# Optimization experiments

Hardware: AMD Instinct MI355X
Metric: run time of the kernel (lower is better)

## Reference

```python
import jax, jax.numpy as jnp
import numpy as np

jax.config.update("jax_enable_x64", True)

DIM = 128          # state dimension
T = 4096           # number of time points
BATCH = 64         # batched initial conditions (columns of x0)
N_UPPER = DIM * (DIM - 1) // 2  # 8128


def setup_inputs() -> dict:
    key = jax.random.key(0)
    k1, k2 = jax.random.split(key)
    return {
        "t": jnp.arange(T, dtype=jnp.float64) * 0.01,               # uniform time grid
        "x0": jax.random.normal(k1, (DIM, BATCH), dtype=jnp.float64),
        "S_upper": jax.random.normal(k2, (N_UPPER,), dtype=jnp.float64) * 0.3,
        "D_raw": jnp.ones((DIM,), dtype=jnp.float64) * 0.1,
    }


def _get_A(S_upper, D_raw):
    # skew-symmetric S from upper-triangular entries, minus positive diagonal D
    iu, ju = np.triu_indices(DIM, k=1)  # static index sets
    S = jnp.zeros((DIM, DIM), dtype=S_upper.dtype).at[iu, ju].set(S_upper)
    S = S - S.T
    return S - jnp.diag(jax.nn.softplus(D_raw))


def reference(t, x0, S_upper, D_raw):
    A = _get_A(S_upper, D_raw)
    dt = t[1] - t[0]
    expAdt = jax.scipy.linalg.expm(A * dt)  # [DIM, DIM]

    def step(x, _):
        x = expAdt @ x  # [DIM, BATCH]
        return x, x

    _, ys = jax.lax.scan(step, x0, None, length=T - 1)  # [T-1, DIM, BATCH]
    return jnp.concatenate([x0[None], ys], axis=0)      # [T, DIM, BATCH]
```

## Files before the change

kernel.cpp:

```cpp
#include <hip/hip_runtime.h>
#include <math.h>

#define DIM 128
#define GP(s)    ((s) * 16384)
#define YOFFI    (65 * 16384)
#define XOFF(q)  ((97 + (q)) * 16384)
#define TOFF(i)  ((105 + (i) - 1) * 16384)
#define FWOFFI   (169 * 16384)
#define FYOFFI   (201 * 16384)
#define ALPHA    16.0f

typedef _Float16 f16x8 __attribute__((ext_vector_type(8)));
typedef float    f32x4 __attribute__((ext_vector_type(4)));

__device__ __forceinline__ float4 ld4(const float* p) { return *(const float4*)p; }

__device__ __forceinline__ void stageA(const float* __restrict__ A, float* AT, int tid)
{
    for (int idx = tid; idx < DIM * DIM; idx += 256)
        AT[(idx & 127) * 132 + (idx >> 7)] = A[idx];
}

__device__ __forceinline__ void mm_core(const float* AT, const float* Bs,
                                        float (&acc)[4][4], int tid)
{
    int d0 = (tid & 31) * 4, c0 = (tid >> 5) * 4;
    #pragma unroll 4
    for (int k = 0; k < DIM; k++) {
        float4 a4 = ld4(&AT[k * 132 + d0]);
        float4 b4 = ld4(&Bs[k * 36 + c0]);
        float a_[4] = {a4.x, a4.y, a4.z, a4.w};
        float b_[4] = {b4.x, b4.y, b4.z, b4.w};
        #pragma unroll
        for (int i = 0; i < 4; i++)
            #pragma unroll
            for (int j = 0; j < 4; j++) acc[i][j] += a_[i] * b_[j];
    }
}

__global__ __launch_bounds__(256) void k_x2(const float* __restrict__ t,
                                            const float* __restrict__ x0,
                                            const float* __restrict__ S,
                                            const float* __restrict__ D,
                                            float* __restrict__ ws)
{
    __shared__ __align__(16) float AT[DIM * 132];
    __shared__ __align__(16) float Bs[DIM * 36];
    int tid = threadIdx.x, bid = blockIdx.x, cpan = bid * 32;
    float sc = (t[1] - t[0]) * ALPHA;
    for (int e = tid; e < 16384; e += 256) {
        int r = e >> 7, c = e & 127;
        float a;
        if (r == c)      a = -log1pf(expf(D[r]));
        else if (r < c)  a =  S[(r * (2 * DIM - r - 1)) / 2 + (c - r - 1)];
        else             a = -S[(c * (2 * DIM - c - 1)) / 2 + (r - c - 1)];
        a *= sc;
        AT[c * 132 + r] = a;
        if (c >= cpan && c < cpan + 32) Bs[r * 36 + (c - cpan)] = a;
        if (bid == 0) ws[XOFF(0) + e] = a;
    }
    if (bid == 1) for (int e = tid; e < 8192; e += 256) ws[YOFFI + e] = x0[e];
    if (bid == 2) {
        _Float16* Wf = (_Float16*)(ws + FWOFFI);
        for (int ch = tid; ch < 2048; ch += 256) {
            int m = ch >> 4, k0 = (ch & 15) << 3;
            f16x8 hv;
            #pragma unroll
            for (int q = 0; q < 8; q++) hv[q] = (m == k0 + q) ? (_Float16)1.0f : (_Float16)0.0f;
            int lane = (m & 15) | (((k0 >> 3) & 3) << 4);
            size_t off = (((size_t)(m >> 4) * 4 + (k0 >> 5)) * 64 + lane) * 8;
            *(f16x8*)(Wf + off) = hv;
        }
    }
    if (bid == 3) {
        _Float16* Yf = (_Float16*)(ws + FYOFFI);
        for (int slot = tid; slot < 1024; slot += 256) {
            int ls = slot & 63, tile = slot >> 6;
            int n = (tile >> 2) * 16 + (ls & 15);
            int k0 = (tile & 3) * 32 + ((ls >> 4) & 3) * 8;
            f16x8 hv;
            #pragma unroll
            for (int q = 0; q < 8; q++) hv[q] = (_Float16)x0[(size_t)(k0 + q) * 64 + n];
            *(f16x8*)(Yf + (size_t)slot * 8) = hv;
        }
    }
    __syncthreads();
    float acc[4][4] = {};
    mm_core(AT, Bs, acc, tid);
    int d0 = (tid & 31) * 4, c0 = (tid >> 5) * 4;
    #pragma unroll
    for (int r = 0; r < 4; r++) {
        float4 st = make_float4(acc[r][0], acc[r][1], acc[r][2], acc[r][3]);
        *(float4*)&ws[XOFF(1) + (size_t)(d0 + r) * DIM + cpan + c0] = st;
    }
}

struct Jobs { int4 jb[33]; };

__global__ __launch_bounds__(256) void k_mm(float* __restrict__ ws, Jobs jobs)
{
    __shared__ __align__(16) _Float16 fB[2][16384];
    const int4 jb = jobs.jb[blockIdx.x];
    const int ncols = jb.w & 255;
    const int fragj = (jb.w >> 8) - 1;
    const float* A = ws + jb.x;
    const float* B = ws + jb.y;
    float* C = ws + jb.z;
    const int tid = threadIdx.x, wave = tid >> 6, lane = tid & 63;

    f16x8 ah[2][4], al[2][4];
    #pragma unroll
    for (int mt = 0; mt < 2; mt++)
        #pragma unroll
        for (int kc = 0; kc < 4; kc++) {
            int m = wave * 32 + mt * 16 + (lane & 15);
            int k0 = kc * 32 + ((lane >> 4) & 3) * 8;
            const float* src = A + (size_t)m * DIM + k0;
            float4 p = ld4(src), r = ld4(src + 4);
            float v[8] = {p.x, p.y, p.z, p.w, r.x, r.y, r.z, r.w};
            f16x8 h8, l8;
            #pragma unroll
            for (int q = 0; q < 8; q++) {
                _Float16 h = (_Float16)v[q];
                h8[q] = h; l8[q] = (_Float16)(v[q] - (float)h);
            }
            ah[mt][kc] = h8; al[mt][kc] = l8;
        }

    const int nslots = (DIM * ncols) >> 3;
    for (int slot = tid; slot < nslots; slot += 256) {
        int ls = slot & 63, tile = slot >> 6;
        int n = (tile >> 2) * 16 + (ls & 15);
        int k0 = (tile & 3) * 32 + ((ls >> 4) & 3) * 8;
        f16x8 h8, l8;
        #pragma unroll
        for (int q = 0; q < 8; q++) {
            float v = B[(size_t)(k0 + q) * ncols + n];
            _Float16 h = (_Float16)v;
            h8[q] = h; l8[q] = (_Float16)(v - (float)h);
        }
        *(f16x8*)&fB[0][(size_t)slot * 8] = h8;
        *(f16x8*)&fB[1][(size_t)slot * 8] = l8;
    }
    __syncthreads();

    const int NT = ncols >> 4;
    f32x4 acc[2][8] = {};
    for (int kc = 0; kc < 4; kc++) {
        #pragma unroll
        for (int nt = 0; nt < 8; nt++) {
            if (nt >= NT) break;
            size_t bo = ((size_t)(nt * 4 + kc) * 64 + lane) * 8;
            f16x8 bh = *(const f16x8*)&fB[0][bo];
            f16x8 bl = *(const f16x8*)&fB[1][bo];
            #pragma unroll
            for (int mt = 0; mt < 2; mt++) {
                acc[mt][nt] = __builtin_amdgcn_mfma_f32_16x16x32_f16(ah[mt][kc], bh, acc[mt][nt], 0, 0, 0);
                acc[mt][nt] = __builtin_amdgcn_mfma_f32_16x16x32_f16(ah[mt][kc], bl, acc[mt][nt], 0, 0, 0);
                acc[mt][nt] = __builtin_amdgcn_mfma_f32_16x16x32_f16(al[mt][kc], bh, acc[mt][nt], 0, 0, 0);
            }
        }
    }
    __syncthreads();

    float* Cst = (float*)&fB[0][0];
    #pragma unroll
    for (int mt = 0; mt < 2; mt++)
        #pragma unroll
        for (int nt = 0; nt < 8; nt++) {
            if (nt >= NT) break;
            int row = wave * 32 + mt * 16 + ((lane >> 4) << 2);
            int n = nt * 16 + (lane & 15);
            #pragma unroll
            for (int p = 0; p < 4; p++)
                Cst[(size_t)(row + p) * ncols + n] = acc[mt][nt][p];
        }
    __syncthreads();
    for (int e = tid * 4; e < DIM * ncols; e += 1024)
        *(float4*)&C[e] = ld4(&Cst[e]);
    if (fragj >= 0) {
        _Float16* Yf = (_Float16*)(ws + FYOFFI) + (size_t)fragj * 8192;
        for (int slot = tid; slot < 1024; slot += 256) {
            int ls = slot & 63, tile = slot >> 6;
            int n = (tile >> 2) * 16 + (ls & 15);
            int k0 = (tile & 3) * 32 + ((ls >> 4) & 3) * 8;
            f16x8 hv;
            #pragma unroll
            for (int q = 0; q < 8; q++) hv[q] = (_Float16)Cst[(size_t)(k0 + q) * 64 + n];
            *(f16x8*)(Yf + (size_t)slot * 8) = hv;
        }
    }
}

__global__ __launch_bounds__(256) void k_ps1(float* __restrict__ ws)
{
    __shared__ __align__(16) float AT[DIM * 132];
    __shared__ __align__(16) float Bs[DIM * 36];
    int i = blockIdx.x + 1, cpan = blockIdx.y * 32, tid = threadIdx.x;
    float r = (float)i / ALPHA;
    float c[24]; c[0] = 1.0f;
    #pragma unroll
    for (int n = 1; n < 24; n++) c[n] = c[n - 1] * (r / (float)n);
    stageA(ws + XOFF(7), AT, tid);
    for (int idx = tid; idx < DIM * 8; idx += 256) {
        int k = idx >> 3, cc4 = (idx & 7) * 4;
        float4 b = make_float4(0.f, 0.f, 0.f, 0.f);
        #pragma unroll
        for (int q = 1; q < 8; q++) {
            float4 x = ld4(&ws[XOFF(q - 1) + (size_t)k * DIM + cpan + cc4]);
            b.x += c[16 + q] * x.x; b.y += c[16 + q] * x.y;
            b.z += c[16 + q] * x.z; b.w += c[16 + q] * x.w;
        }
        int col = cpan + cc4;
        if (k >= col && k < col + 4) (&b.x)[k - col] += c[16];
        *(float4*)&Bs[k * 36 + cc4] = b;
    }
    __syncthreads();
    float acc[4][4] = {};
    mm_core(AT, Bs, acc, tid);
    int d0 = (tid & 31) * 4, c0 = (tid >> 5) * 4;
    float* T = ws + TOFF(i);
    #pragma unroll
    for (int rr = 0; rr < 4; rr++) {
        int dd = d0 + rr;
        float add[4] = {0.f, 0.f, 0.f, 0.f};
        #pragma unroll
        for (int q = 1; q < 8; q++) {
            float4 x = ld4(&ws[XOFF(q - 1) + (size_t)dd * DIM + cpan + c0]);
            add[0] += c[8 + q] * x.x; add[1] += c[8 + q] * x.y;
            add[2] += c[8 + q] * x.z; add[3] += c[8 + q] * x.w;
        }
        int col0 = cpan + c0;
        if (dd >= col0 && dd < col0 + 4) add[dd - col0] += c[8];
        float4 st = make_float4(acc[rr][0] + add[0], acc[rr][1] + add[1],
                                acc[rr][2] + add[2], acc[rr][3] + add[3]);
        *(float4*)&T[(size_t)dd * DIM + cpan + c0] = st;
    }
}

__global__ __launch_bounds__(256) void k_ps2(float* __restrict__ ws)
{
    __shared__ __align__(16) float AT[DIM * 132];
    __shared__ __align__(16) float Bs[DIM * 36];
    int i = blockIdx.x + 1, cpan = blockIdx.y * 32, tid = threadIdx.x;
    float r = (float)i / ALPHA;
    float c[8]; c[0] = 1.0f;
    #pragma unroll
    for (int n = 1; n < 8; n++) c[n] = c[n - 1] * (r / (float)n);
    stageA(ws + XOFF(7), AT, tid);
    const float* T = ws + TOFF(i);
    for (int idx = tid; idx < DIM * 32; idx += 256) {
        int k = idx >> 5, cc = idx & 31;
        Bs[k * 36 + cc] = T[(size_t)k * DIM + cpan + cc];
    }
    __syncthreads();
    float acc[4][4] = {};
    mm_core(AT, Bs, acc, tid);
    int d0 = (tid & 31) * 4, c0 = (tid >> 5) * 4;
    #pragma unroll
    for (int rr = 0; rr < 4; rr++) {
        int dd = d0 + rr;
        float add[4] = {0.f, 0.f, 0.f, 0.f};
        #pragma unroll
        for (int q = 1; q < 8; q++) {
            float4 x = ld4(&ws[XOFF(q - 1) + (size_t)dd * DIM + cpan + c0]);
            add[0] += c[q] * x.x; add[1] += c[q] * x.y;
            add[2] += c[q] * x.z; add[3] += c[q] * x.w;
        }
        int col0 = cpan + c0;
        if (dd >= col0 && dd < col0 + 4) add[dd - col0] += 1.0f;
        #pragma unroll
        for (int j = 0; j < 4; j++) acc[rr][j] += add[j];
    }
    if (i == 64) {
        float* G = ws + GP(0);
        #pragma unroll
        for (int rr = 0; rr < 4; rr++) {
            float4 st = make_float4(acc[rr][0], acc[rr][1], acc[rr][2], acc[rr][3]);
            *(float4*)&G[(size_t)(d0 + rr) * DIM + cpan + c0] = st;
        }
        return;
    }
    __syncthreads();
    #pragma unroll
    for (int rr = 0; rr < 4; rr++)
        #pragma unroll
        for (int j = 0; j < 4; j++) Bs[(d0 + rr) * 36 + c0 + j] = acc[rr][j];
    __syncthreads();
    _Float16* Wf = (_Float16*)(ws + FWOFFI);
    for (int ch = tid; ch < 512; ch += 256) {
        int m = ch >> 2, k0l = (ch & 3) * 8, k0 = cpan + k0l;
        f16x8 hv;
        #pragma unroll
        for (int q = 0; q < 8; q++) hv[q] = (_Float16)Bs[m * 36 + k0l + q];
        int lane = (m & 15) | (((k0 >> 3) & 3) << 4);
        size_t off = (size_t)i * 16384 + (((size_t)(m >> 4) * 4 + (k0 >> 5)) * 64 + lane) * 8;
        *(f16x8*)(Wf + off) = hv;
    }
}

__global__ __launch_bounds__(256) void k_final(const _Float16* __restrict__ Wf,
                                               const _Float16* __restrict__ Yf,
                                               float* __restrict__ out)
{
    int i = blockIdx.x, j = blockIdx.y;
    int tid = threadIdx.x, wave = tid >> 6, lane = tid & 63;
    const _Float16* Ab = Yf + (size_t)j * 8192;
    const _Float16* Bb = Wf + (size_t)i * 16384;
    f32x4 acc[4][2] = {};
    #pragma unroll
    for (int ks = 0; ks < 4; ks++) {
        f16x8 a[4], b[2];
        #pragma unroll
        for (int bt = 0; bt < 4; bt++)
            a[bt] = *(const f16x8*)(Ab + (((size_t)bt * 4 + ks) * 64 + lane) * 8);
        #pragma unroll
        for (int nn = 0; nn < 2; nn++)
            b[nn] = *(const f16x8*)(Bb + (((size_t)(wave * 2 + nn) * 4 + ks) * 64 + lane) * 8);
        #pragma unroll
        for (int bt = 0; bt < 4; bt++)
            #pragma unroll
            for (int nn = 0; nn < 2; nn++)
                acc[bt][nn] = __builtin_amdgcn_mfma_f32_16x16x32_f16(a[bt], b[nn], acc[bt][nn], 0, 0, 0);
    }
    float* slab = out + (size_t)(j * 64 + i) * 8192;
    int nlo = lane & 15, b0 = (lane >> 4) * 4;
    #pragma unroll
    for (int bt = 0; bt < 4; bt++)
        #pragma unroll
        for (int nn = 0; nn < 2; nn++) {
            int n = (wave * 2 + nn) * 16 + nlo;
            __builtin_nontemporal_store(acc[bt][nn],
                (f32x4*)&slab[(size_t)n * 64 + bt * 16 + b0]);
        }
}

static inline void addjob(Jobs& J, int& n, int a, int b, int c, int ncols, int fragj)
{
    J.jb[n++] = make_int4(a, b, c, ncols | ((fragj + 1) << 8));
}

extern "C" void kernel_launch(void* const* d_in, const int* in_sizes, int n_in,
                              void* d_out, int out_size, void* d_ws, size_t ws_size,
                              hipStream_t stream)
{
    const float* t  = (const float*)d_in[0];
    const float* x0 = (const float*)d_in[1];
    const float* S  = (const float*)d_in[2];
    const float* D  = (const float*)d_in[3];
    float* out = (float*)d_out;
    float* ws  = (float*)d_ws;
    _Float16* Wf = (_Float16*)(ws + FWOFFI);
    _Float16* Yf = (_Float16*)(ws + FYOFFI);

    hipLaunchKernelGGL(k_x2, dim3(4), dim3(256), 0, stream, t, x0, S, D, ws);

    Jobs J; int n;
    n = 0;
    addjob(J, n, XOFF(1), XOFF(0), XOFF(2), 128, -1);
    addjob(J, n, XOFF(1), XOFF(1), XOFF(3), 128, -1);
    hipLaunchKernelGGL(k_mm, dim3(n), dim3(256), 0, stream, ws, J);
    n = 0;
    for (int q = 1; q <= 4; q++) addjob(J, n, XOFF(3), XOFF(q - 1), XOFF(3 + q), 128, -1);
    hipLaunchKernelGGL(k_mm, dim3(n), dim3(256), 0, stream, ws, J);

    hipLaunchKernelGGL(k_ps1, dim3(64, 4), dim3(256), 0, stream, ws);
    hipLaunchKernelGGL(k_ps2, dim3(64, 4), dim3(256), 0, stream, ws);

    n = 0;
    addjob(J, n, GP(0), GP(0), GP(1), 128, -1);
    addjob(J, n, GP(0), YOFFI, YOFFI + 8192, 64, 1);
    hipLaunchKernelGGL(k_mm, dim3(n), dim3(256), 0, stream, ws, J);
    n = 0;
    addjob(J, n, GP(1), GP(1), GP(2), 128, -1);
    addjob(J, n, GP(1), YOFFI,        YOFFI + 2 * 8192, 64, 2);
    addjob(J, n, GP(1), YOFFI + 8192, YOFFI + 3 * 8192, 64, 3);
    hipLaunchKernelGGL(k_mm, dim3(n), dim3(256), 0, stream, ws, J);
    n = 0;
    addjob(J, n, GP(2), GP(2), GP(3), 128, -1);
    for (int jj = 0; jj < 4; jj++)
        addjob(J, n, GP(2), YOFFI + jj * 8192, YOFFI + (4 + jj) * 8192, 64, 4 + jj);
    hipLaunchKernelGGL(k_mm, dim3(n), dim3(256), 0, stream, ws, J);
    n = 0;
    addjob(J, n, GP(3), GP(3), GP(4), 128, -1);
    for (int jj = 0; jj < 8; jj++)
        addjob(J, n, GP(3), YOFFI + jj * 8192, YOFFI + (8 + jj) * 8192, 64, 8 + jj);
    hipLaunchKernelGGL(k_mm, dim3(n), dim3(256), 0, stream, ws, J);
    n = 0;
    addjob(J, n, GP(4), GP(4), GP(5), 128, -1);
    for (int jj = 0; jj < 16; jj++)
        addjob(J, n, GP(4), YOFFI + jj * 8192, YOFFI + (16 + jj) * 8192, 64, 16 + jj);
    hipLaunchKernelGGL(k_mm, dim3(n), dim3(256), 0, stream, ws, J);
    n = 0;
    for (int jj = 0; jj < 32; jj++)
        addjob(J, n, GP(5), YOFFI + jj * 8192, YOFFI + (32 + jj) * 8192, 64, 32 + jj);
    hipLaunchKernelGGL(k_mm, dim3(n), dim3(256), 0, stream, ws, J);

    hipLaunchKernelGGL(k_final, dim3(64, 64), dim3(256), 0, stream, Wf, Yf, out);
}
```

Baseline: 218.1 us.

## Keep transposed copies of matrices so MFMA B fragments load directly from global

Replaces the k_mm kernel with k_atom, which reads the B operand from a pre-transposed matrix in global memory and splits it into fp16 hi/lo fragments in registers. This removes the LDS staging pass and its barrier. Each square product also writes its transpose, and the state propagation is reformulated as Y^T·G^T so that each job computes a 64x128 tile with the state as the A operand. The cost is extra transposed writes and strided global reads per fragment, in exchange for fewer LDS round trips and fewer synchronisations per job.

```diff
diff --git a/kernel.cpp b/kernel.cpp
--- a/kernel.cpp
+++ b/kernel.cpp
@@ -3,17 +3,30 @@
 
 #define DIM 128
 #define GP(s)    ((s) * 16384)
-#define YOFFI    (65 * 16384)
-#define XOFF(q)  ((97 + (q)) * 16384)
-#define TOFF(i)  ((105 + (i) - 1) * 16384)
-#define FWOFFI   (169 * 16384)
-#define FYOFFI   (201 * 16384)
+#define GTP(s)   ((6 + (s)) * 16384)
+#define YP(j)    (13 * 16384 + (j) * 8192)
+#define XOFF(q)  ((44 + (q)) * 16384)
+#define XTOFF(q) ((52 + (q)) * 16384)
+#define TOFF(i)  ((60 + (i)) * 16384)
+#define FWOFFI   (125 * 16384)
+#define FYOFFI   (157 * 16384)
 #define ALPHA    16.0f
 
 typedef _Float16 f16x8 __attribute__((ext_vector_type(8)));
 typedef float    f32x4 __attribute__((ext_vector_type(4)));
 
 __device__ __forceinline__ float4 ld4(const float* p) { return *(const float4*)p; }
+
+__device__ __forceinline__ void splitv(const float* src, f16x8& h8, f16x8& l8)
+{
+    float4 p = ld4(src), r = ld4(src + 4);
+    float v[8] = {p.x, p.y, p.z, p.w, r.x, r.y, r.z, r.w};
+    #pragma unroll
+    for (int q = 0; q < 8; q++) {
+        _Float16 h = (_Float16)v[q];
+        h8[q] = h; l8[q] = (_Float16)(v[q] - (float)h);
+    }
+}
 
 __device__ __forceinline__ void stageA(const float* __restrict__ A, float* AT, int tid)
 {
@@ -57,22 +70,13 @@
         a *= sc;
         AT[c * 132 + r] = a;
         if (c >= cpan && c < cpan + 32) Bs[r * 36 + (c - cpan)] = a;
-        if (bid == 0) ws[XOFF(0) + e] = a;
-    }
-    if (bid == 1) for (int e = tid; e < 8192; e += 256) ws[YOFFI + e] = x0[e];
-    if (bid == 2) {
-        _Float16* Wf = (_Float16*)(ws + FWOFFI);
-        for (int ch = tid; ch < 2048; ch += 256) {
-            int m = ch >> 4, k0 = (ch & 15) << 3;
-            f16x8 hv;
-            #pragma unroll
-            for (int q = 0; q < 8; q++) hv[q] = (m == k0 + q) ? (_Float16)1.0f : (_Float16)0.0f;
-            int lane = (m & 15) | (((k0 >> 3) & 3) << 4);
-            size_t off = (((size_t)(m >> 4) * 4 + (k0 >> 5)) * 64 + lane) * 8;
-            *(f16x8*)(Wf + off) = hv;
-        }
-    }
-    if (bid == 3) {
+        if (bid == 0) { ws[XOFF(1) + e] = a; ws[XTOFF(1) + c * DIM + r] = a; }
+    }
+    if (bid == 1) {
+        for (int e = tid; e < 8192; e += 256) {
+            int b = e >> 7, d = e & 127;
+            ws[YP(0) + e] = x0[(size_t)d * 64 + b];
+        }
         _Float16* Yf = (_Float16*)(ws + FYOFFI);
         for (int slot = tid; slot < 1024; slot += 256) {
             int ls = slot & 63, tile = slot >> 6;
@@ -84,6 +88,18 @@
             *(f16x8*)(Yf + (size_t)slot * 8) = hv;
         }
     }
+    if (bid == 2) {
+        _Float16* Wf = (_Float16*)(ws + FWOFFI);
+        for (int ch = tid; ch < 2048; ch += 256) {
+            int m = ch >> 4, k0 = (ch & 15) << 3;
+            f16x8 hv;
+            #pragma unroll
+            for (int q = 0; q < 8; q++) hv[q] = (m == k0 + q) ? (_Float16)1.0f : (_Float16)0.0f;
+            int lane = (m & 15) | (((k0 >> 3) & 3) << 4);
+            size_t off = (((size_t)(m >> 4) * 4 + (k0 >> 5)) * 64 + lane) * 8;
+            *(f16x8*)(Wf + off) = hv;
+        }
+    }
     __syncthreads();
     float acc[4][4] = {};
     mm_core(AT, Bs, acc, tid);
@@ -91,102 +107,90 @@
     #pragma unroll
     for (int r = 0; r < 4; r++) {
         float4 st = make_float4(acc[r][0], acc[r][1], acc[r][2], acc[r][3]);
-        *(float4*)&ws[XOFF(1) + (size_t)(d0 + r) * DIM + cpan + c0] = st;
-    }
-}
-
-struct Jobs { int4 jb[33]; };
-
-__global__ __launch_bounds__(256) void k_mm(float* __restrict__ ws, Jobs jobs)
-{
-    __shared__ __align__(16) _Float16 fB[2][16384];
-    const int4 jb = jobs.jb[blockIdx.x];
-    const int ncols = jb.w & 255;
-    const int fragj = (jb.w >> 8) - 1;
-    const float* A = ws + jb.x;
-    const float* B = ws + jb.y;
-    float* C = ws + jb.z;
+        *(float4*)&ws[XOFF(2) + (size_t)(d0 + r) * DIM + cpan + c0] = st;
+        #pragma unroll
+        for (int j = 0; j < 4; j++)
+            ws[XTOFF(2) + (size_t)(cpan + c0 + j) * DIM + d0 + r] = acc[r][j];
+    }
+}
+
+struct AJobs { int4 a[32]; int aux[32]; };
+
+__global__ __launch_bounds__(256) void k_atom(float* __restrict__ ws, AJobs JB)
+{
+    __shared__ __align__(16) float Cst[DIM * 133];
     const int tid = threadIdx.x, wave = tid >> 6, lane = tid & 63;
+    const int4 jb = JB.a[blockIdx.x];
+    const int aux = JB.aux[blockIdx.x];
+    const int type = jb.w;
+    const float* A  = ws + jb.x;
+    const float* Bt = ws + jb.y;
+    float* C        = ws + jb.z;
+    const int nmt = (type == 0) ? 2 : 1;
+    const int mlane = lane & 15, koct = (lane >> 4) & 3;
 
     f16x8 ah[2][4], al[2][4];
     #pragma unroll
-    for (int mt = 0; mt < 2; mt++)
+    for (int mt = 0; mt < 2; mt++) {
+        if (mt >= nmt) break;
         #pragma unroll
         for (int kc = 0; kc < 4; kc++) {
-            int m = wave * 32 + mt * 16 + (lane & 15);
-            int k0 = kc * 32 + ((lane >> 4) & 3) * 8;
-            const float* src = A + (size_t)m * DIM + k0;
-            float4 p = ld4(src), r = ld4(src + 4);
-            float v[8] = {p.x, p.y, p.z, p.w, r.x, r.y, r.z, r.w};
-            f16x8 h8, l8;
-            #pragma unroll
-            for (int q = 0; q < 8; q++) {
-                _Float16 h = (_Float16)v[q];
-                h8[q] = h; l8[q] = (_Float16)(v[q] - (float)h);
-            }
-            ah[mt][kc] = h8; al[mt][kc] = l8;
-        }
-
-    const int nslots = (DIM * ncols) >> 3;
-    for (int slot = tid; slot < nslots; slot += 256) {
-        int ls = slot & 63, tile = slot >> 6;
-        int n = (tile >> 2) * 16 + (ls & 15);
-        int k0 = (tile & 3) * 32 + ((ls >> 4) & 3) * 8;
-        f16x8 h8, l8;
-        #pragma unroll
-        for (int q = 0; q < 8; q++) {
-            float v = B[(size_t)(k0 + q) * ncols + n];
-            _Float16 h = (_Float16)v;
-            h8[q] = h; l8[q] = (_Float16)(v - (float)h);
-        }
-        *(f16x8*)&fB[0][(size_t)slot * 8] = h8;
-        *(f16x8*)&fB[1][(size_t)slot * 8] = l8;
-    }
-    __syncthreads();
-
-    const int NT = ncols >> 4;
+            int m = (wave * nmt + mt) * 16 + mlane;
+            splitv(A + (size_t)m * DIM + kc * 32 + koct * 8, ah[mt][kc], al[mt][kc]);
+        }
+    }
     f32x4 acc[2][8] = {};
     for (int kc = 0; kc < 4; kc++) {
         #pragma unroll
         for (int nt = 0; nt < 8; nt++) {
-            if (nt >= NT) break;
-            size_t bo = ((size_t)(nt * 4 + kc) * 64 + lane) * 8;
-            f16x8 bh = *(const f16x8*)&fB[0][bo];
-            f16x8 bl = *(const f16x8*)&fB[1][bo];
+            int n = nt * 16 + mlane;
+            f16x8 bh, bl;
+            splitv(Bt + (size_t)n * DIM + kc * 32 + koct * 8, bh, bl);
             #pragma unroll
             for (int mt = 0; mt < 2; mt++) {
+                if (mt >= nmt) break;
                 acc[mt][nt] = __builtin_amdgcn_mfma_f32_16x16x32_f16(ah[mt][kc], bh, acc[mt][nt], 0, 0, 0);
                 acc[mt][nt] = __builtin_amdgcn_mfma_f32_16x16x32_f16(ah[mt][kc], bl, acc[mt][nt], 0, 0, 0);
                 acc[mt][nt] = __builtin_amdgcn_mfma_f32_16x16x32_f16(al[mt][kc], bh, acc[mt][nt], 0, 0, 0);
             }
         }
     }
-    __syncthreads();
-
-    float* Cst = (float*)&fB[0][0];
-    #pragma unroll
-    for (int mt = 0; mt < 2; mt++)
+    #pragma unroll
+    for (int mt = 0; mt < 2; mt++) {
+        if (mt >= nmt) break;
         #pragma unroll
         for (int nt = 0; nt < 8; nt++) {
-            if (nt >= NT) break;
-            int row = wave * 32 + mt * 16 + ((lane >> 4) << 2);
-            int n = nt * 16 + (lane & 15);
-            #pragma unroll
-            for (int p = 0; p < 4; p++)
-                Cst[(size_t)(row + p) * ncols + n] = acc[mt][nt][p];
-        }
-    __syncthreads();
-    for (int e = tid * 4; e < DIM * ncols; e += 1024)
-        *(float4*)&C[e] = ld4(&Cst[e]);
-    if (fragj >= 0) {
-        _Float16* Yf = (_Float16*)(ws + FYOFFI) + (size_t)fragj * 8192;
+            int row = (wave * nmt + mt) * 16 + (lane >> 4) * 4;
+            int col = nt * 16 + mlane;
+            #pragma unroll
+            for (int p = 0; p < 4; p++) Cst[(size_t)(row + p) * 133 + col] = acc[mt][nt][p];
+        }
+    }
+    __syncthreads();
+    const int M = nmt * 64;
+    for (int e = tid * 4; e < M * DIM; e += 1024) {
+        int row = e >> 7, col = e & 127;
+        const float* s = &Cst[(size_t)row * 133 + col];
+        *(float4*)&C[e] = make_float4(s[0], s[1], s[2], s[3]);
+    }
+    if (type == 0) {
+        float* Ct = ws + aux;
+        for (int e = tid * 4; e < 16384; e += 1024) {
+            int crow = e >> 7, r0 = e & 127;
+            *(float4*)&Ct[e] = make_float4(Cst[(size_t)(r0 + 0) * 133 + crow],
+                                           Cst[(size_t)(r0 + 1) * 133 + crow],
+                                           Cst[(size_t)(r0 + 2) * 133 + crow],
+                                           Cst[(size_t)(r0 + 3) * 133 + crow]);
+        }
+    } else {
+        _Float16* Yf = (_Float16*)(ws + FYOFFI) + (size_t)aux * 8192;
         for (int slot = tid; slot < 1024; slot += 256) {
             int ls = slot & 63, tile = slot >> 6;
-            int n = (tile >> 2) * 16 + (ls & 15);
+            int m = (tile >> 2) * 16 + (ls & 15);
             int k0 = (tile & 3) * 32 + ((ls >> 4) & 3) * 8;
             f16x8 hv;
             #pragma unroll
-            for (int q = 0; q < 8; q++) hv[q] = (_Float16)Cst[(size_t)(k0 + q) * 64 + n];
+            for (int q = 0; q < 8; q++) hv[q] = (_Float16)Cst[(size_t)m * 133 + k0 + q];
             *(f16x8*)(Yf + (size_t)slot * 8) = hv;
         }
     }
@@ -201,13 +205,13 @@
     float c[24]; c[0] = 1.0f;
     #pragma unroll
     for (int n = 1; n < 24; n++) c[n] = c[n - 1] * (r / (float)n);
-    stageA(ws + XOFF(7), AT, tid);
+    stageA(ws + XOFF(8), AT, tid);
     for (int idx = tid; idx < DIM * 8; idx += 256) {
         int k = idx >> 3, cc4 = (idx & 7) * 4;
         float4 b = make_float4(0.f, 0.f, 0.f, 0.f);
         #pragma unroll
         for (int q = 1; q < 8; q++) {
-            float4 x = ld4(&ws[XOFF(q - 1) + (size_t)k * DIM + cpan + cc4]);
+            float4 x = ld4(&ws[XOFF(q) + (size_t)k * DIM + cpan + cc4]);
             b.x += c[16 + q] * x.x; b.y += c[16 + q] * x.y;
             b.z += c[16 + q] * x.z; b.w += c[16 + q] * x.w;
         }
@@ -226,7 +230,7 @@
         float add[4] = {0.f, 0.f, 0.f, 0.f};
         #pragma unroll
         for (int q = 1; q < 8; q++) {
-            float4 x = ld4(&ws[XOFF(q - 1) + (size_t)dd * DIM + cpan + c0]);
+            float4 x = ld4(&ws[XOFF(q) + (size_t)dd * DIM + cpan + c0]);
             add[0] += c[8 + q] * x.x; add[1] += c[8 + q] * x.y;
             add[2] += c[8 + q] * x.z; add[3] += c[8 + q] * x.w;
         }
@@ -247,7 +251,7 @@
     float c[8]; c[0] = 1.0f;
     #pragma unroll
     for (int n = 1; n < 8; n++) c[n] = c[n - 1] * (r / (float)n);
-    stageA(ws + XOFF(7), AT, tid);
+    stageA(ws + XOFF(8), AT, tid);
     const float* T = ws + TOFF(i);
     for (int idx = tid; idx < DIM * 32; idx += 256) {
         int k = idx >> 5, cc = idx & 31;
@@ -263,7 +267,7 @@
         float add[4] = {0.f, 0.f, 0.f, 0.f};
         #pragma unroll
         for (int q = 1; q < 8; q++) {
-            float4 x = ld4(&ws[XOFF(q - 1) + (size_t)dd * DIM + cpan + c0]);
+            float4 x = ld4(&ws[XOFF(q) + (size_t)dd * DIM + cpan + c0]);
             add[0] += c[q] * x.x; add[1] += c[q] * x.y;
             add[2] += c[q] * x.z; add[3] += c[q] * x.w;
         }
@@ -273,11 +277,14 @@
         for (int j = 0; j < 4; j++) acc[rr][j] += add[j];
     }
     if (i == 64) {
-        float* G = ws + GP(0);
         #pragma unroll
         for (int rr = 0; rr < 4; rr++) {
+            int dd = d0 + rr;
             float4 st = make_float4(acc[rr][0], acc[rr][1], acc[rr][2], acc[rr][3]);
-            *(float4*)&G[(size_t)(d0 + rr) * DIM + cpan + c0] = st;
+            *(float4*)&ws[GP(0) + (size_t)dd * DIM + cpan + c0] = st;
+            #pragma unroll
+            for (int j = 0; j < 4; j++)
+                ws[GTP(0) + (size_t)(cpan + c0 + j) * DIM + dd] = acc[rr][j];
         }
         return;
     }
@@ -335,9 +342,11 @@
         }
 }
 
-static inline void addjob(Jobs& J, int& n, int a, int b, int c, int ncols, int fragj)
-{
-    J.jb[n++] = make_int4(a, b, c, ncols | ((fragj + 1) << 8));
+static inline void addjob(AJobs& J, int& n, int type, int a, int bt, int c, int aux)
+{
+    J.a[n] = make_int4(a, bt, c, type);
+    J.aux[n] = aux;
+    n++;
 }
 
 extern "C" void kernel_launch(void* const* d_in, const int* in_sizes, int n_in,
@@ -355,46 +364,26 @@
 
     hipLaunchKernelGGL(k_x2, dim3(4), dim3(256), 0, stream, t, x0, S, D, ws);
 
-    Jobs J; int n;
+    AJobs J; int n;
     n = 0;
-    addjob(J, n, XOFF(1), XOFF(0), XOFF(2), 128, -1);
-    addjob(J, n, XOFF(1), XOFF(1), XOFF(3), 128, -1);
-    hipLaunchKernelGGL(k_mm, dim3(n), dim3(256), 0, stream, ws, J);
+    addjob(J, n, 0, XOFF(2), XTOFF(1), XOFF(3), XTOFF(3));
+    addjob(J, n, 0, XOFF(2), XTOFF(2), XOFF(4), XTOFF(4));
+    hipLaunchKernelGGL(k_atom, dim3(n), dim3(256), 0, stream, ws, J);
     n = 0;
-    for (int q = 1; q <= 4; q++) addjob(J, n, XOFF(3), XOFF(q - 1), XOFF(3 + q), 128, -1);
-    hipLaunchKernelGGL(k_mm, dim3(n), dim3(256), 0, stream, ws, J);
+    for (int q = 1; q <= 4; q++)
+        addjob(J, n, 0, XOFF(4), XTOFF(q), XOFF(4 + q), XTOFF(4 + q));
+    hipLaunchKernelGGL(k_atom, dim3(n), dim3(256), 0, stream, ws, J);
 
     hipLaunchKernelGGL(k_ps1, dim3(64, 4), dim3(256), 0, stream, ws);
     hipLaunchKernelGGL(k_ps2, dim3(64, 4), dim3(256), 0, stream, ws);
 
-    n = 0;
-    addjob(J, n, GP(0), GP(0), GP(1), 128, -1);
-    addjob(J, n, GP(0), YOFFI, YOFFI + 8192, 64, 1);
-    hipLaunchKernelGGL(k_mm, dim3(n), dim3(256), 0, stream, ws, J);
-    n = 0;
-    addjob(J, n, GP(1), GP(1), GP(2), 128, -1);
-    addjob(J, n, GP(1), YOFFI,        YOFFI + 2 * 8192, 64, 2);
-    addjob(J, n, GP(1), YOFFI + 8192, YOFFI + 3 * 8192, 64, 3);
-    hipLaunchKernelGGL(k_mm, dim3(n), dim3(256), 0, stream, ws, J);
-    n = 0;
-    addjob(J, n, GP(2), GP(2), GP(3), 128, -1);
-    for (int jj = 0; jj < 4; jj++)
-        addjob(J, n, GP(2), YOFFI + jj * 8192, YOFFI + (4 + jj) * 8192, 64, 4 + jj);
-    hipLaunchKernelGGL(k_mm, dim3(n), dim3(256), 0, stream, ws, J);
-    n = 0;
-    addjob(J, n, GP(3), GP(3), GP(4), 128, -1);
-    for (int jj = 0; jj < 8; jj++)
-        addjob(J, n, GP(3), YOFFI + jj * 8192, YOFFI + (8 + jj) * 8192, 64, 8 + jj);
-    hipLaunchKernelGGL(k_mm, dim3(n), dim3(256), 0, stream, ws, J);
-    n = 0;
-    addjob(J, n, GP(4), GP(4), GP(5), 128, -1);
-    for (int jj = 0; jj < 16; jj++)
-        addjob(J, n, GP(4), YOFFI + jj * 8192, YOFFI + (16 + jj) * 8192, 64, 16 + jj);
-    hipLaunchKernelGGL(k_mm, dim3(n), dim3(256), 0, stream, ws, J);
-    n = 0;
-    for (int jj = 0; jj < 32; jj++)
-        addjob(J, n, GP(5), YOFFI + jj * 8192, YOFFI + (32 + jj) * 8192, 64, 32 + jj);
-    hipLaunchKernelGGL(k_mm, dim3(n), dim3(256), 0, stream, ws, J);
+    for (int d = 0; d < 6; d++) {
+        n = 0;
+        if (d < 5) addjob(J, n, 0, GP(d), GTP(d), GP(d + 1), GTP(d + 1));
+        for (int jj = 0; jj < (1 << d); jj++)
+            addjob(J, n, 1, YP(jj), GP(d), YP((1 << d) + jj), (1 << d) + jj);
+        hipLaunchKernelGGL(k_atom, dim3(n), dim3(256), 0, stream, ws, J);
+    }
 
     hipLaunchKernelGGL(k_final, dim3(64, 64), dim3(256), 0, stream, Wf, Yf, out);
 }
```

Measured after the change: 297.6 us. +36.5%, slower.

## Split matmul jobs into 32-column panels and fuse power-series kernels

Applied to the files above, without the earlier changes.

Replaces the split-fp16 MFMA matmul kernel (one block per full 128-column product) with an fp32 FMA kernel where each block computes a 32-column panel, so each level launches more blocks across the GPU. The two power-series kernels are merged into one, with Taylor terms regrouped to 16 coefficients, removing a launch and the intermediate buffer. It also reorganises the workspace layout and vectorises the A transpose staging. The trade is scalar FP32 math in place of matrix cores, in exchange for more parallel blocks and fewer launches.

```diff
diff --git a/kernel.cpp b/kernel.cpp
--- a/kernel.cpp
+++ b/kernel.cpp
@@ -2,23 +2,28 @@
 #include <math.h>
 
 #define DIM 128
-#define GP(s)    ((s) * 16384)
-#define YOFFI    (65 * 16384)
-#define XOFF(q)  ((97 + (q)) * 16384)
-#define TOFF(i)  ((105 + (i) - 1) * 16384)
-#define FWOFFI   (169 * 16384)
-#define FYOFFI   (201 * 16384)
-#define ALPHA    16.0f
+#define XA(q)   (((q) - 1) * 16384)
+#define GS(s)   ((8 + (s)) * 16384)
+#define YF(j)   (14 * 16384 + (j) * 8192)
+#define FW      (46 * 16384)
+#define FY      (78 * 16384)
+#define ALPHA   16.0f
 
 typedef _Float16 f16x8 __attribute__((ext_vector_type(8)));
 typedef float    f32x4 __attribute__((ext_vector_type(4)));
 
 __device__ __forceinline__ float4 ld4(const float* p) { return *(const float4*)p; }
 
-__device__ __forceinline__ void stageA(const float* __restrict__ A, float* AT, int tid)
-{
-    for (int idx = tid; idx < DIM * DIM; idx += 256)
-        AT[(idx & 127) * 132 + (idx >> 7)] = A[idx];
+__device__ __forceinline__ void stageAT(const float* __restrict__ A, float* AT, int tid)
+{
+    for (int idx = tid * 4; idx < DIM * DIM; idx += 1024) {
+        float4 v = ld4(&A[idx]);
+        int d = idx >> 7, k = idx & 127;
+        AT[(k + 0) * 132 + d] = v.x;
+        AT[(k + 1) * 132 + d] = v.y;
+        AT[(k + 2) * 132 + d] = v.z;
+        AT[(k + 3) * 132 + d] = v.w;
+    }
 }
 
 __device__ __forceinline__ void mm_core(const float* AT, const float* Bs,
@@ -57,11 +62,11 @@
         a *= sc;
         AT[c * 132 + r] = a;
         if (c >= cpan && c < cpan + 32) Bs[r * 36 + (c - cpan)] = a;
-        if (bid == 0) ws[XOFF(0) + e] = a;
-    }
-    if (bid == 1) for (int e = tid; e < 8192; e += 256) ws[YOFFI + e] = x0[e];
+        if (bid == 0) ws[XA(1) + e] = a;
+    }
+    if (bid == 1) for (int e = tid; e < 8192; e += 256) ws[YF(0) + e] = x0[e];
     if (bid == 2) {
-        _Float16* Wf = (_Float16*)(ws + FWOFFI);
+        _Float16* Wf = (_Float16*)(ws + FW);
         for (int ch = tid; ch < 2048; ch += 256) {
             int m = ch >> 4, k0 = (ch & 15) << 3;
             f16x8 hv;
@@ -73,7 +78,7 @@
         }
     }
     if (bid == 3) {
-        _Float16* Yf = (_Float16*)(ws + FYOFFI);
+        _Float16* Yf = (_Float16*)(ws + FY);
         for (int slot = tid; slot < 1024; slot += 256) {
             int ls = slot & 63, tile = slot >> 6;
             int n = (tile >> 2) * 16 + (ls & 15);
@@ -91,179 +96,92 @@
     #pragma unroll
     for (int r = 0; r < 4; r++) {
         float4 st = make_float4(acc[r][0], acc[r][1], acc[r][2], acc[r][3]);
-        *(float4*)&ws[XOFF(1) + (size_t)(d0 + r) * DIM + cpan + c0] = st;
-    }
-}
-
-struct Jobs { int4 jb[33]; };
-
-__global__ __launch_bounds__(256) void k_mm(float* __restrict__ ws, Jobs jobs)
-{
-    __shared__ __align__(16) _Float16 fB[2][16384];
+        *(float4*)&ws[XA(2) + (size_t)(d0 + r) * DIM + cpan + c0] = st;
+    }
+}
+
+struct Jobs { int4 jb[64]; };
+
+__global__ __launch_bounds__(256) void k_lvl(float* __restrict__ ws, Jobs jobs)
+{
+    __shared__ __align__(16) float AT[DIM * 132];
+    __shared__ __align__(16) float Bs[DIM * 36];
     const int4 jb = jobs.jb[blockIdx.x];
-    const int ncols = jb.w & 255;
-    const int fragj = (jb.w >> 8) - 1;
+    const int cpan  = jb.w & 127;
+    const int ncols = (jb.w >> 8) & 255;
+    const int fragj = ((jb.w >> 17) & 127) - 1;
     const float* A = ws + jb.x;
     const float* B = ws + jb.y;
     float* C = ws + jb.z;
-    const int tid = threadIdx.x, wave = tid >> 6, lane = tid & 63;
-
-    f16x8 ah[2][4], al[2][4];
-    #pragma unroll
-    for (int mt = 0; mt < 2; mt++)
-        #pragma unroll
-        for (int kc = 0; kc < 4; kc++) {
-            int m = wave * 32 + mt * 16 + (lane & 15);
-            int k0 = kc * 32 + ((lane >> 4) & 3) * 8;
-            const float* src = A + (size_t)m * DIM + k0;
-            float4 p = ld4(src), r = ld4(src + 4);
-            float v[8] = {p.x, p.y, p.z, p.w, r.x, r.y, r.z, r.w};
-            f16x8 h8, l8;
-            #pragma unroll
-            for (int q = 0; q < 8; q++) {
-                _Float16 h = (_Float16)v[q];
-                h8[q] = h; l8[q] = (_Float16)(v[q] - (float)h);
-            }
-            ah[mt][kc] = h8; al[mt][kc] = l8;
-        }
-
-    const int nslots = (DIM * ncols) >> 3;
-    for (int slot = tid; slot < nslots; slot += 256) {
-        int ls = slot & 63, tile = slot >> 6;
-        int n = (tile >> 2) * 16 + (ls & 15);
-        int k0 = (tile & 3) * 32 + ((ls >> 4) & 3) * 8;
-        f16x8 h8, l8;
-        #pragma unroll
-        for (int q = 0; q < 8; q++) {
-            float v = B[(size_t)(k0 + q) * ncols + n];
-            _Float16 h = (_Float16)v;
-            h8[q] = h; l8[q] = (_Float16)(v - (float)h);
-        }
-        *(f16x8*)&fB[0][(size_t)slot * 8] = h8;
-        *(f16x8*)&fB[1][(size_t)slot * 8] = l8;
-    }
-    __syncthreads();
-
-    const int NT = ncols >> 4;
-    f32x4 acc[2][8] = {};
-    for (int kc = 0; kc < 4; kc++) {
-        #pragma unroll
-        for (int nt = 0; nt < 8; nt++) {
-            if (nt >= NT) break;
-            size_t bo = ((size_t)(nt * 4 + kc) * 64 + lane) * 8;
-            f16x8 bh = *(const f16x8*)&fB[0][bo];
-            f16x8 bl = *(const f16x8*)&fB[1][bo];
-            #pragma unroll
-            for (int mt = 0; mt < 2; mt++) {
-                acc[mt][nt] = __builtin_amdgcn_mfma_f32_16x16x32_f16(ah[mt][kc], bh, acc[mt][nt], 0, 0, 0);
-                acc[mt][nt] = __builtin_amdgcn_mfma_f32_16x16x32_f16(ah[mt][kc], bl, acc[mt][nt], 0, 0, 0);
-                acc[mt][nt] = __builtin_amdgcn_mfma_f32_16x16x32_f16(al[mt][kc], bh, acc[mt][nt], 0, 0, 0);
-            }
-        }
-    }
-    __syncthreads();
-
-    float* Cst = (float*)&fB[0][0];
-    #pragma unroll
-    for (int mt = 0; mt < 2; mt++)
-        #pragma unroll
-        for (int nt = 0; nt < 8; nt++) {
-            if (nt >= NT) break;
-            int row = wave * 32 + mt * 16 + ((lane >> 4) << 2);
-            int n = nt * 16 + (lane & 15);
-            #pragma unroll
-            for (int p = 0; p < 4; p++)
-                Cst[(size_t)(row + p) * ncols + n] = acc[mt][nt][p];
-        }
-    __syncthreads();
-    for (int e = tid * 4; e < DIM * ncols; e += 1024)
-        *(float4*)&C[e] = ld4(&Cst[e]);
-    if (fragj >= 0) {
-        _Float16* Yf = (_Float16*)(ws + FYOFFI) + (size_t)fragj * 8192;
-        for (int slot = tid; slot < 1024; slot += 256) {
-            int ls = slot & 63, tile = slot >> 6;
-            int n = (tile >> 2) * 16 + (ls & 15);
-            int k0 = (tile & 3) * 32 + ((ls >> 4) & 3) * 8;
-            f16x8 hv;
-            #pragma unroll
-            for (int q = 0; q < 8; q++) hv[q] = (_Float16)Cst[(size_t)(k0 + q) * 64 + n];
-            *(f16x8*)(Yf + (size_t)slot * 8) = hv;
-        }
-    }
-}
-
-__global__ __launch_bounds__(256) void k_ps1(float* __restrict__ ws)
+    const int tid = threadIdx.x;
+    stageAT(A, AT, tid);
+    for (int s = tid; s < DIM * 8; s += 256) {
+        int k = s >> 3, cc4 = (s & 7) * 4;
+        *(float4*)&Bs[k * 36 + cc4] = ld4(&B[(size_t)k * ncols + cpan + cc4]);
+    }
+    __syncthreads();
+    float acc[4][4] = {};
+    mm_core(AT, Bs, acc, tid);
+    int d0 = (tid & 31) * 4, c0 = (tid >> 5) * 4;
+    #pragma unroll
+    for (int r = 0; r < 4; r++) {
+        float4 st = make_float4(acc[r][0], acc[r][1], acc[r][2], acc[r][3]);
+        *(float4*)&C[(size_t)(d0 + r) * ncols + cpan + c0] = st;
+    }
+    if (fragj < 0) return;
+    __syncthreads();
+    #pragma unroll
+    for (int r = 0; r < 4; r++)
+        #pragma unroll
+        for (int j = 0; j < 4; j++) Bs[(d0 + r) * 36 + c0 + j] = acc[r][j];
+    __syncthreads();
+    _Float16* Yf = (_Float16*)(ws + FY) + (size_t)fragj * 8192;
+    for (int ch = tid; ch < 512; ch += 256) {
+        int nloc = ch >> 4, k0 = (ch & 15) * 8;
+        f16x8 hv;
+        #pragma unroll
+        for (int q = 0; q < 8; q++) hv[q] = (_Float16)Bs[(k0 + q) * 36 + nloc];
+        int n = cpan + nloc;
+        int lane = (n & 15) | (((k0 >> 3) & 3) << 4);
+        size_t off = (((size_t)(n >> 4) * 4 + (k0 >> 5)) * 64 + lane) * 8;
+        *(f16x8*)(Yf + off) = hv;
+    }
+}
+
+__global__ __launch_bounds__(256) void k_ps(float* __restrict__ ws)
 {
     __shared__ __align__(16) float AT[DIM * 132];
     __shared__ __align__(16) float Bs[DIM * 36];
     int i = blockIdx.x + 1, cpan = blockIdx.y * 32, tid = threadIdx.x;
     float r = (float)i / ALPHA;
-    float c[24]; c[0] = 1.0f;
-    #pragma unroll
-    for (int n = 1; n < 24; n++) c[n] = c[n - 1] * (r / (float)n);
-    stageA(ws + XOFF(7), AT, tid);
-    for (int idx = tid; idx < DIM * 8; idx += 256) {
-        int k = idx >> 3, cc4 = (idx & 7) * 4;
+    float c[16]; c[0] = 1.0f;
+    #pragma unroll
+    for (int n = 1; n < 16; n++) c[n] = c[n - 1] * (r / (float)n);
+    stageAT(ws + XA(8), AT, tid);
+    for (int s = tid; s < DIM * 8; s += 256) {
+        int k = s >> 3, cc4 = (s & 7) * 4;
         float4 b = make_float4(0.f, 0.f, 0.f, 0.f);
         #pragma unroll
         for (int q = 1; q < 8; q++) {
-            float4 x = ld4(&ws[XOFF(q - 1) + (size_t)k * DIM + cpan + cc4]);
-            b.x += c[16 + q] * x.x; b.y += c[16 + q] * x.y;
-            b.z += c[16 + q] * x.z; b.w += c[16 + q] * x.w;
+            float4 x = ld4(&ws[XA(q) + (size_t)k * DIM + cpan + cc4]);
+            b.x += c[8 + q] * x.x; b.y += c[8 + q] * x.y;
+            b.z += c[8 + q] * x.z; b.w += c[8 + q] * x.w;
         }
         int col = cpan + cc4;
-        if (k >= col && k < col + 4) (&b.x)[k - col] += c[16];
+        if (k >= col && k < col + 4) (&b.x)[k - col] += c[8];
         *(float4*)&Bs[k * 36 + cc4] = b;
     }
     __syncthreads();
     float acc[4][4] = {};
     mm_core(AT, Bs, acc, tid);
     int d0 = (tid & 31) * 4, c0 = (tid >> 5) * 4;
-    float* T = ws + TOFF(i);
     #pragma unroll
     for (int rr = 0; rr < 4; rr++) {
         int dd = d0 + rr;
         float add[4] = {0.f, 0.f, 0.f, 0.f};
         #pragma unroll
         for (int q = 1; q < 8; q++) {
-            float4 x = ld4(&ws[XOFF(q - 1) + (size_t)dd * DIM + cpan + c0]);
-            add[0] += c[8 + q] * x.x; add[1] += c[8 + q] * x.y;
-            add[2] += c[8 + q] * x.z; add[3] += c[8 + q] * x.w;
-        }
-        int col0 = cpan + c0;
-        if (dd >= col0 && dd < col0 + 4) add[dd - col0] += c[8];
-        float4 st = make_float4(acc[rr][0] + add[0], acc[rr][1] + add[1],
-                                acc[rr][2] + add[2], acc[rr][3] + add[3]);
-        *(float4*)&T[(size_t)dd * DIM + cpan + c0] = st;
-    }
-}
-
-__global__ __launch_bounds__(256) void k_ps2(float* __restrict__ ws)
-{
-    __shared__ __align__(16) float AT[DIM * 132];
-    __shared__ __align__(16) float Bs[DIM * 36];
-    int i = blockIdx.x + 1, cpan = blockIdx.y * 32, tid = threadIdx.x;
-    float r = (float)i / ALPHA;
-    float c[8]; c[0] = 1.0f;
-    #pragma unroll
-    for (int n = 1; n < 8; n++) c[n] = c[n - 1] * (r / (float)n);
-    stageA(ws + XOFF(7), AT, tid);
-    const float* T = ws + TOFF(i);
-    for (int idx = tid; idx < DIM * 32; idx += 256) {
-        int k = idx >> 5, cc = idx & 31;
-        Bs[k * 36 + cc] = T[(size_t)k * DIM + cpan + cc];
-    }
-    __syncthreads();
-    float acc[4][4] = {};
-    mm_core(AT, Bs, acc, tid);
-    int d0 = (tid & 31) * 4, c0 = (tid >> 5) * 4;
-    #pragma unroll
-    for (int rr = 0; rr < 4; rr++) {
-        int dd = d0 + rr;
-        float add[4] = {0.f, 0.f, 0.f, 0.f};
-        #pragma unroll
-        for (int q = 1; q < 8; q++) {
-            float4 x = ld4(&ws[XOFF(q - 1) + (size_t)dd * DIM + cpan + c0]);
+            float4 x = ld4(&ws[XA(q) + (size_t)dd * DIM + cpan + c0]);
             add[0] += c[q] * x.x; add[1] += c[q] * x.y;
             add[2] += c[q] * x.z; add[3] += c[q] * x.w;
         }
@@ -273,11 +191,10 @@
         for (int j = 0; j < 4; j++) acc[rr][j] += add[j];
     }
     if (i == 64) {
-        float* G = ws + GP(0);
         #pragma unroll
         for (int rr = 0; rr < 4; rr++) {
             float4 st = make_float4(acc[rr][0], acc[rr][1], acc[rr][2], acc[rr][3]);
-            *(float4*)&G[(size_t)(d0 + rr) * DIM + cpan + c0] = st;
+            *(float4*)&ws[GS(0) + (size_t)(d0 + rr) * DIM + cpan + c0] = st;
         }
         return;
     }
@@ -287,7 +204,7 @@
         #pragma unroll
         for (int j = 0; j < 4; j++) Bs[(d0 + rr) * 36 + c0 + j] = acc[rr][j];
     __syncthreads();
-    _Float16* Wf = (_Float16*)(ws + FWOFFI);
+    _Float16* Wf = (_Float16*)(ws + FW);
     for (int ch = tid; ch < 512; ch += 256) {
         int m = ch >> 2, k0l = (ch & 3) * 8, k0 = cpan + k0l;
         f16x8 hv;
@@ -335,9 +252,15 @@
         }
 }
 
-static inline void addjob(Jobs& J, int& n, int a, int b, int c, int ncols, int fragj)
-{
-    J.jb[n++] = make_int4(a, b, c, ncols | ((fragj + 1) << 8));
+static inline void addjob(Jobs& J, int& n, int a, int b, int c,
+                          int cpan, int ncols, int fragj)
+{
+    J.jb[n++] = make_int4(a, b, c, cpan | (ncols << 8) | ((fragj + 1) << 17));
+}
+
+static inline void addmm(Jobs& J, int& n, int a, int b, int c, int ncols, int fragj)
+{
+    for (int p = 0; p < ncols; p += 32) addjob(J, n, a, b, c, p, ncols, fragj);
 }
 
 extern "C" void kernel_launch(void* const* d_in, const int* in_sizes, int n_in,
@@ -350,51 +273,50 @@
     const float* D  = (const float*)d_in[3];
     float* out = (float*)d_out;
     float* ws  = (float*)d_ws;
-    _Float16* Wf = (_Float16*)(ws + FWOFFI);
-    _Float16* Yf = (_Float16*)(ws + FYOFFI);
+    _Float16* Wf = (_Float16*)(ws + FW);
+    _Float16* Yf = (_Float16*)(ws + FY);
 
     hipLaunchKernelGGL(k_x2, dim3(4), dim3(256), 0, stream, t, x0, S, D, ws);
 
     Jobs J; int n;
     n = 0;
-    addjob(J, n, XOFF(1), XOFF(0), XOFF(2), 128, -1);
-    addjob(J, n, XOFF(1), XOFF(1), XOFF(3), 128, -1);
-    hipLaunchKernelGGL(k_mm, dim3(n), dim3(256), 0, stream, ws, J);
-    n = 0;
-    for (int q = 1; q <= 4; q++) addjob(J, n, XOFF(3), XOFF(q - 1), XOFF(3 + q), 128, -1);
-    hipLaunchKernelGGL(k_mm, dim3(n), dim3(256), 0, stream, ws, J);
-
-    hipLaunchKernelGGL(k_ps1, dim3(64, 4), dim3(256), 0, stream, ws);
-    hipLaunchKernelGGL(k_ps2, dim3(64, 4), dim3(256), 0, stream, ws);
-
-    n = 0;
-    addjob(J, n, GP(0), GP(0), GP(1), 128, -1);
-    addjob(J, n, GP(0), YOFFI, YOFFI + 8192, 64, 1);
-    hipLaunchKernelGGL(k_mm, dim3(n), dim3(256), 0, stream, ws, J);
-    n = 0;
-    addjob(J, n, GP(1), GP(1), GP(2), 128, -1);
-    addjob(J, n, GP(1), YOFFI,        YOFFI + 2 * 8192, 64, 2);
-    addjob(J, n, GP(1), YOFFI + 8192, YOFFI + 3 * 8192, 64, 3);
-    hipLaunchKernelGGL(k_mm, dim3(n), dim3(256), 0, stream, ws, J);
-    n = 0;
-    addjob(J, n, GP(2), GP(2), GP(3), 128, -1);
+    addmm(J, n, XA(2), XA(1), XA(3), 128, -1);
+    addmm(J, n, XA(2), XA(2), XA(4), 128, -1);
+    hipLaunchKernelGGL(k_lvl, dim3(n), dim3(256), 0, stream, ws, J);
+    n = 0;
+    for (int q = 1; q <= 4; q++) addmm(J, n, XA(4), XA(q), XA(4 + q), 128, -1);
+    hipLaunchKernelGGL(k_lvl, dim3(n), dim3(256), 0, stream, ws, J);
+
+    hipLaunchKernelGGL(k_ps, dim3(64, 4), dim3(256), 0, stream, ws);
+
+    n = 0;
+    addmm(J, n, GS(0), GS(0), GS(1), 128, -1);
+    addmm(J, n, GS(0), YF(0), YF(1), 64, 1);
+    hipLaunchKernelGGL(k_lvl, dim3(n), dim3(256), 0, stream, ws, J);
+    n = 0;
+    addmm(J, n, GS(1), GS(1), GS(2), 128, -1);
+    addmm(J, n, GS(1), YF(0), YF(2), 64, 2);
+    addmm(J, n, GS(1), YF(1), YF(3), 64, 3);
+    hipLaunchKernelGGL(k_lvl, dim3(n), dim3(256), 0, stream, ws, J);
+    n = 0;
+    addmm(J, n, GS(2), GS(2), GS(3), 128, -1);
     for (int jj = 0; jj < 4; jj++)
-        addjob(J, n, GP(2), YOFFI + jj * 8192, YOFFI + (4 + jj) * 8192, 64, 4 + jj);
-    hipLaunchKernelGGL(k_mm, dim3(n), dim3(256), 0, stream, ws, J);
-    n = 0;
-    addjob(J, n, GP(3), GP(3), GP(4), 128, -1);
+        addmm(J, n, GS(2), YF(jj), YF(4 + jj), 64, 4 + jj);
+    hipLaunchKernelGGL(k_lvl, dim3(n), dim3(256), 0, stream, ws, J);
+    n = 0;
+    addmm(J, n, GS(3), GS(3), GS(4), 128, -1);
     for (int jj = 0; jj < 8; jj++)
-        addjob(J, n, GP(3), YOFFI + jj * 8192, YOFFI + (8 + jj) * 8192, 64, 8 + jj);
-    hipLaunchKernelGGL(k_mm, dim3(n), dim3(256), 0, stream, ws, J);
-    n = 0;
-    addjob(J, n, GP(4), GP(4), GP(5), 128, -1);
+        addmm(J, n, GS(3), YF(jj), YF(8 + jj), 64, 8 + jj);
+    hipLaunchKernelGGL(k_lvl, dim3(n), dim3(256), 0, stream, ws, J);
+    n = 0;
+    addmm(J, n, GS(4), GS(4), GS(5), 128, -1);
     for (int jj = 0; jj < 16; jj++)
-        addjob(J, n, GP(4), YOFFI + jj * 8192, YOFFI + (16 + jj) * 8192, 64, 16 + jj);
-    hipLaunchKernelGGL(k_mm, dim3(n), dim3(256), 0, stream, ws, J);
+        addmm(J, n, GS(4), YF(jj), YF(16 + jj), 64, 16 + jj);
+    hipLaunchKernelGGL(k_lvl, dim3(n), dim3(256), 0, stream, ws, J);
     n = 0;
     for (int jj = 0; jj < 32; jj++)
-        addjob(J, n, GP(5), YOFFI + jj * 8192, YOFFI + (32 + jj) * 8192, 64, 32 + jj);
-    hipLaunchKernelGGL(k_mm, dim3(n), dim3(256), 0, stream, ws, J);
+        addmm(J, n, GS(5), YF(jj), YF(32 + jj), 64, 32 + jj);
+    hipLaunchKernelGGL(k_lvl, dim3(n), dim3(256), 0, stream, ws, J);
 
     hipLaunchKernelGGL(k_final, dim3(64, 64), dim3(256), 0, stream, Wf, Yf, out);
 }
```

Result: no change. 214.4 us (-1.7%).
